# Kernel optimization log

Measured on AMD Instinct MI355X. Metric: run time of the kernel, lower is better.

## Reference

```python
import jax, jax.numpy as jnp
import numpy as np

IMG = 224
WS = 8      # windows_size
STRIDE = 2
M = 1

def _dct_mat(size):
    i = np.arange(size)[:, None]
    j = np.arange(size)[None, :]
    scale = np.where(i == 0, np.sqrt(1.0 / size), np.sqrt(2.0 / size))
    return (scale * np.cos((j + 0.5) * np.pi * i / size)).astype(np.float32)

def _gen_filter(start, end, size):
    i = np.arange(size)[:, None]
    j = np.arange(size)[None, :]
    s = i + j
    return np.where((s > end) | (s < start), 0.0, 1.0).astype(np.float32)

def setup_inputs() -> dict:
    key = jax.random.key(0)
    x = jax.random.normal(key, (16, 3, IMG, IMG), dtype=jnp.float32)
    D = jnp.asarray(_dct_mat(WS))                       # [ws, ws] DCT matrix
    filt = jnp.asarray(_gen_filter(WS // 3, WS * 2, WS))  # high-pass base filter
    return {"x": x, "D": D, "filt": filt}

def reference(x, D, filt):
    b, c, H, W = x.shape
    n = (H - WS) // STRIDE + 1                 # patches per side (109)
    rows = jnp.arange(n)[:, None] * STRIDE + jnp.arange(WS)[None, :]  # [n, ws]
    # unfold: overlapping stride-2 patches -> [b, n, n, c, ws, ws]
    p = x[:, :, rows, :]                       # [b, c, n, ws, W]
    p = p[..., rows]                           # [b, c, n, ws, n, ws]
    p = p.transpose(0, 2, 4, 1, 3, 5)          # [b, n, n, c, ws, ws]
    # block DCT: D @ p @ D^T
    xd = jnp.einsum('pi,bmncij,qj->bmncpq', D, p, D)
    # filter (use_learnable=False, norm=False -> plain elementwise mask)
    y = xd * filt
    # block IDCT: D^T @ y @ D
    y = jnp.einsum('pi,bmncpq,qj->bmncij', D, y, D)
    # fold: overlap-add scatter back to [b, c, H, W]
    hh = rows[:, None, :, None]                # [n,1,ws,1]
    ww = rows[None, :, None, :]                # [1,n,1,ws]
    flat = hh * W + ww                         # [n,n,ws,ws] flat spatial index
    y_t = y.transpose(0, 3, 1, 2, 4, 5)        # [b, c, n, n, ws, ws]
    out = jnp.zeros((b, c, H * W), x.dtype).at[:, :, flat].add(y_t)
    return out.reshape(b, c, H, W)             # m=1 -> cat is identity
```

## Files before the change

kernel.cpp:

```cpp
#include <hip/hip_runtime.h>

#define IMG 224
#define NP 109
#define BC 48
#define NPIX (IMG * IMG)
#define TILE 56
#define QT 28
#define PT 31
#define XR 68
#define XC2 34
#define NTHR 512


#define LOAD_D_SCALARS(D)                                                  \
    const float d0_0 = (D)[0], d0_1 = (D)[1], d0_2 = (D)[2], d0_3 = (D)[3],\
                d0_4 = (D)[4], d0_5 = (D)[5], d0_6 = (D)[6], d0_7 = (D)[7];\
    const float d1_0 = (D)[8],  d1_1 = (D)[9],  d1_2 = (D)[10],            \
                d1_3 = (D)[11], d1_4 = (D)[12], d1_5 = (D)[13],            \
                d1_6 = (D)[14], d1_7 = (D)[15];

#define O_XE   0
#define O_XO   (O_XE + XR * XC2)
#define O_RS   (O_XO + XR * XC2)
#define O_RT   (O_RS + XR * PT)
#define O_RSE  O_RS
#define O_RSO  (O_RSE + PT * QT)
#define O_RTE  (O_RSO + PT * QT)
#define O_RTO  (O_RTE + PT * QT)
#define O_CA   (O_RT + XR * PT)
#define O_CB   (O_CA + PT * PT)
#define O_CC   (O_CB + PT * PT)
#define LDS_FLOATS (O_CC + PT * PT)

__global__ __launch_bounds__(NTHR) void fused_dct_kernel(
    const float* __restrict__ x, const float* __restrict__ D,
    const float* __restrict__ filt, float* __restrict__ out)
{
    __shared__ float lds[LDS_FLOATS];
    float* const xe_s = lds + O_XE;
    float* const xo_s = lds + O_XO;
    float* const rs_s = lds + O_RS;
    float* const rt_s = lds + O_RT;
    float* const ca_s = lds + O_CA;
    float* const cb_s = lds + O_CB;
    float* const cc_s = lds + O_CC;
    float* const RSe  = lds + O_RSE;
    float* const RSo  = lds + O_RSO;
    float* const RTe  = lds + O_RTE;
    float* const RTo  = lds + O_RTO;

    const int tid = threadIdx.x;
    const int h0 = blockIdx.y * TILE;
    const int w0 = blockIdx.x * TILE;
    const int bc = blockIdx.z;

    LOAD_D_SCALARS(D)
    const float w00 = 1.0f - filt[0];
    const float w01 = 1.0f - filt[1];
    const float w10 = 1.0f - filt[8];

    const float* xb = x + (size_t)bc * NPIX;

    for (int i = tid; i < XR * XC2; i += NTHR) {
        int r  = i / XC2;
        int c2 = i - r * XC2;
        int gr = h0 - 6 + r;
        int gc = w0 - 6 + 2 * c2;
        float2 v = make_float2(0.f, 0.f);
        if ((unsigned)gr < (unsigned)IMG && (unsigned)gc < (unsigned)IMG)
            v = *(const float2*)(xb + (size_t)gr * IMG + gc);
        xe_s[r * XC2 + c2] = v.x;
        xo_s[r * XC2 + c2] = v.y;
    }
    __syncthreads();

    for (int i = tid; i < XR * PT; i += NTHR) {
        int r  = i / PT;
        int pc = i - r * PT;
        int b  = r * XC2 + pc;
        float e0 = xe_s[b],     o0 = xo_s[b];
        float e1 = xe_s[b + 1], o1 = xo_s[b + 1];
        float e2 = xe_s[b + 2], o2 = xo_s[b + 2];
        float e3 = xe_s[b + 3], o3 = xo_s[b + 3];
        float s = fmaf(e0, d0_0, fmaf(o0, d0_1,
                  fmaf(e1, d0_2, fmaf(o1, d0_3,
                  fmaf(e2, d0_4, fmaf(o2, d0_5,
                  fmaf(e3, d0_6, o3 * d0_7)))))));
        float t = fmaf(e0, d1_0, fmaf(o0, d1_1,
                  fmaf(e1, d1_2, fmaf(o1, d1_3,
                  fmaf(e2, d1_4, fmaf(o2, d1_5,
                  fmaf(e3, d1_6, o3 * d1_7)))))));
        rs_s[i] = s;
        rt_s[i] = t;
    }
    __syncthreads();

    const int pr0 = (h0 >> 1) - 3;
    const int pc0 = (w0 >> 1) - 3;
    for (int p = tid; p < PT * PT; p += NTHR) {
        int prl = p / PT;
        int pcl = p - prl * PT;
        int b   = (2 * prl) * PT + pcl;
        float c00 = 0.f, c01 = 0.f, c10 = 0.f;
#define P3_ROW(i)                                                              \
        {                                                                      \
            float s = rs_s[b + (i) * PT];                                      \
            float t = rt_s[b + (i) * PT];                                      \
            c00 = fmaf(d0_##i, s, c00);                                        \
            c01 = fmaf(d0_##i, t, c01);                                        \
            c10 = fmaf(d1_##i, s, c10);                                        \
        }
        P3_ROW(0) P3_ROW(1) P3_ROW(2) P3_ROW(3)
        P3_ROW(4) P3_ROW(5) P3_ROW(6) P3_ROW(7)
#undef P3_ROW
        bool valid = ((unsigned)(pr0 + prl) < (unsigned)NP) &&
                     ((unsigned)(pc0 + pcl) < (unsigned)NP);
        float m = valid ? 1.0f : 0.0f;
        ca_s[p] = c00 * w00 * m;
        cb_s[p] = c01 * w01 * m;
        cc_s[p] = c10 * w10 * m;
    }
    __syncthreads();

    for (int i = tid; i < PT * QT; i += NTHR) {
        int pr = i / QT;
        int qw = i - pr * QT;
        int b  = pr * PT + qw;
        float se = 0.f, so = 0.f, te = 0.f, to = 0.f;
#define P4_COL(kc, je, jo)                                                     \
        {                                                                      \
            float a = ca_s[b + (kc)];                                          \
            float bb = cb_s[b + (kc)];                                         \
            float c = cc_s[b + (kc)];                                          \
            se = fmaf(a, d0_##je, fmaf(bb, d1_##je, se));                      \
            so = fmaf(a, d0_##jo, fmaf(bb, d1_##jo, so));                      \
            te = fmaf(c, d0_##je, te);                                         \
            to = fmaf(c, d0_##jo, to);                                         \
        }
        P4_COL(0, 6, 7) P4_COL(1, 4, 5) P4_COL(2, 2, 3) P4_COL(3, 0, 1)
#undef P4_COL
        RSe[i] = se; RSo[i] = so; RTe[i] = te; RTo[i] = to;
    }
    __syncthreads();

    const int qh0 = h0 >> 1, qw0 = w0 >> 1;
    float* ob = out + (size_t)bc * NPIX;
    for (int q = tid; q < QT * QT; q += NTHR) {
        int qhl = q / QT;
        int qwl = q - qhl * QT;
        int b   = qhl * QT + qwl;
        float aee = 0.f, aeo = 0.f, aoe = 0.f, aoo = 0.f;
#define P5_ROW(kr, ie, io)                                                     \
        {                                                                      \
            int o = b + (kr) * QT;                                             \
            float se = RSe[o], so = RSo[o], te = RTe[o], to = RTo[o];          \
            aee = fmaf(d0_##ie, se, fmaf(d1_##ie, te, aee));                   \
            aeo = fmaf(d0_##ie, so, fmaf(d1_##ie, to, aeo));                   \
            aoe = fmaf(d0_##io, se, fmaf(d1_##io, te, aoe));                   \
            aoo = fmaf(d0_##io, so, fmaf(d1_##io, to, aoo));                   \
        }
        P5_ROW(0, 6, 7) P5_ROW(1, 4, 5) P5_ROW(2, 2, 3) P5_ROW(3, 0, 1)
#undef P5_ROW

        int qh = qh0 + qhl, qw = qw0 + qwl;
        int nvr = min(qh, NP - 1) - max(qh - 3, 0) + 1;
        int nvc = min(qw, NP - 1) - max(qw - 3, 0) + 1;
        float cnt = (float)(nvr * nvc);

        int xr = (2 * qhl + 6) * XC2 + (qwl + 3);
        float x00 = xe_s[xr],       x01 = xo_s[xr];
        float x10 = xe_s[xr + XC2], x11 = xo_s[xr + XC2];

        float2 o0, o1;
        o0.x = fmaf(cnt, x00, -aee);
        o0.y = fmaf(cnt, x01, -aeo);
        o1.x = fmaf(cnt, x10, -aoe);
        o1.y = fmaf(cnt, x11, -aoo);

        float* orp = ob + (size_t)(h0 + 2 * qhl) * IMG + (w0 + 2 * qwl);
        *(float2*)orp         = o0;
        *(float2*)(orp + IMG) = o1;
    }
}

extern "C" void kernel_launch(void* const* d_in, const int* in_sizes, int n_in,
                              void* d_out, int out_size, void* d_ws, size_t ws_size,
                              hipStream_t stream)
{
    const float* x    = (const float*)d_in[0];
    const float* D    = (const float*)d_in[1];
    const float* filt = (const float*)d_in[2];
    float* out        = (float*)d_out;

    dim3 grid(IMG / TILE, IMG / TILE, BC);
    fused_dct_kernel<<<grid, NTHR, 0, stream>>>(x, D, filt, out);
    (void)d_ws; (void)ws_size;
}
```

Before: 72.60 us.

## Register-block each stage over four outputs with padded LDS and float4 accesses

Each thread of every separable DCT stage now computes four adjacent outputs instead of one. This reuses the overlapping sliding-window inputs held in registers and lets LDS reads and writes and the global stores use float4. LDS rows are padded to multiples of four floats so those vector accesses stay aligned. It cuts LDS instruction count and address arithmetic, at the cost of more registers per thread and fewer threads active in each stage, which may leave much of the 512-thread block idle.

```diff
diff --git a/kernel.cpp b/kernel.cpp
--- a/kernel.cpp
+++ b/kernel.cpp
@@ -9,6 +9,9 @@
 #define PT 31
 #define XR 68
 #define XC2 34
+#define XCP 36
+#define RSP 32
+#define CAP 32
 #define NTHR 512
 
 
@@ -19,24 +22,28 @@
                 d1_3 = (D)[11], d1_4 = (D)[12], d1_5 = (D)[13],            \
                 d1_6 = (D)[14], d1_7 = (D)[15];
 
+#define DOT8(x0,y0,x1,y1,x2,y2,x3,y3, q0,q1,q2,q3,q4,q5,q6,q7)             \
+    fmaf(x0,q0, fmaf(y0,q1, fmaf(x1,q2, fmaf(y1,q3,                        \
+    fmaf(x2,q4, fmaf(y2,q5, fmaf(x3,q6, (y3)*(q7))))))))
+
 #define O_XE   0
-#define O_XO   (O_XE + XR * XC2)
-#define O_RS   (O_XO + XR * XC2)
-#define O_RT   (O_RS + XR * PT)
+#define O_XO   (O_XE + XR * XCP)
+#define O_RS   (O_XO + XR * XCP)
+#define O_RT   (O_RS + XR * RSP)
 #define O_RSE  O_RS
 #define O_RSO  (O_RSE + PT * QT)
 #define O_RTE  (O_RSO + PT * QT)
 #define O_RTO  (O_RTE + PT * QT)
-#define O_CA   (O_RT + XR * PT)
-#define O_CB   (O_CA + PT * PT)
-#define O_CC   (O_CB + PT * PT)
-#define LDS_FLOATS (O_CC + PT * PT)
+#define O_CA   (O_RT + XR * RSP)
+#define O_CB   (O_CA + PT * CAP)
+#define O_CC   (O_CB + PT * CAP)
+#define LDS_FLOATS (O_CC + PT * CAP)
 
 __global__ __launch_bounds__(NTHR) void fused_dct_kernel(
     const float* __restrict__ x, const float* __restrict__ D,
     const float* __restrict__ filt, float* __restrict__ out)
 {
-    __shared__ float lds[LDS_FLOATS];
+    __shared__ __attribute__((aligned(16))) float lds[LDS_FLOATS];
     float* const xe_s = lds + O_XE;
     float* const xo_s = lds + O_XO;
     float* const rs_s = lds + O_RS;
@@ -69,117 +76,172 @@
         float2 v = make_float2(0.f, 0.f);
         if ((unsigned)gr < (unsigned)IMG && (unsigned)gc < (unsigned)IMG)
             v = *(const float2*)(xb + (size_t)gr * IMG + gc);
-        xe_s[r * XC2 + c2] = v.x;
-        xo_s[r * XC2 + c2] = v.y;
-    }
-    __syncthreads();
-
-    for (int i = tid; i < XR * PT; i += NTHR) {
-        int r  = i / PT;
-        int pc = i - r * PT;
-        int b  = r * XC2 + pc;
-        float e0 = xe_s[b],     o0 = xo_s[b];
-        float e1 = xe_s[b + 1], o1 = xo_s[b + 1];
-        float e2 = xe_s[b + 2], o2 = xo_s[b + 2];
-        float e3 = xe_s[b + 3], o3 = xo_s[b + 3];
-        float s = fmaf(e0, d0_0, fmaf(o0, d0_1,
-                  fmaf(e1, d0_2, fmaf(o1, d0_3,
-                  fmaf(e2, d0_4, fmaf(o2, d0_5,
-                  fmaf(e3, d0_6, o3 * d0_7)))))));
-        float t = fmaf(e0, d1_0, fmaf(o0, d1_1,
-                  fmaf(e1, d1_2, fmaf(o1, d1_3,
-                  fmaf(e2, d1_4, fmaf(o2, d1_5,
-                  fmaf(e3, d1_6, o3 * d1_7)))))));
-        rs_s[i] = s;
-        rt_s[i] = t;
+        xe_s[r * XCP + c2] = v.x;
+        xo_s[r * XCP + c2] = v.y;
+    }
+    __syncthreads();
+
+    for (int i = tid; i < XR * 8; i += NTHR) {
+        int r = i >> 3, g = i & 7;
+        int base = r * XCP + 4 * g;
+        float4 E0 = *(const float4*)(xe_s + base);
+        float4 E1 = *(const float4*)(xe_s + base + 4);
+        float4 O0 = *(const float4*)(xo_s + base);
+        float4 O1 = *(const float4*)(xo_s + base + 4);
+        float e0=E0.x, e1=E0.y, e2=E0.z, e3=E0.w, e4=E1.x, e5=E1.y, e6=E1.z;
+        float o0=O0.x, o1=O0.y, o2=O0.z, o3=O0.w, o4=O1.x, o5=O1.y, o6=O1.z;
+        float s0 = DOT8(e0,o0,e1,o1,e2,o2,e3,o3, d0_0,d0_1,d0_2,d0_3,d0_4,d0_5,d0_6,d0_7);
+        float s1 = DOT8(e1,o1,e2,o2,e3,o3,e4,o4, d0_0,d0_1,d0_2,d0_3,d0_4,d0_5,d0_6,d0_7);
+        float s2 = DOT8(e2,o2,e3,o3,e4,o4,e5,o5, d0_0,d0_1,d0_2,d0_3,d0_4,d0_5,d0_6,d0_7);
+        float s3 = DOT8(e3,o3,e4,o4,e5,o5,e6,o6, d0_0,d0_1,d0_2,d0_3,d0_4,d0_5,d0_6,d0_7);
+        float t0 = DOT8(e0,o0,e1,o1,e2,o2,e3,o3, d1_0,d1_1,d1_2,d1_3,d1_4,d1_5,d1_6,d1_7);
+        float t1 = DOT8(e1,o1,e2,o2,e3,o3,e4,o4, d1_0,d1_1,d1_2,d1_3,d1_4,d1_5,d1_6,d1_7);
+        float t2 = DOT8(e2,o2,e3,o3,e4,o4,e5,o5, d1_0,d1_1,d1_2,d1_3,d1_4,d1_5,d1_6,d1_7);
+        float t3 = DOT8(e3,o3,e4,o4,e5,o5,e6,o6, d1_0,d1_1,d1_2,d1_3,d1_4,d1_5,d1_6,d1_7);
+        *(float4*)(rs_s + r * RSP + 4 * g) = make_float4(s0, s1, s2, s3);
+        *(float4*)(rt_s + r * RSP + 4 * g) = make_float4(t0, t1, t2, t3);
     }
     __syncthreads();
 
     const int pr0 = (h0 >> 1) - 3;
     const int pc0 = (w0 >> 1) - 3;
-    for (int p = tid; p < PT * PT; p += NTHR) {
-        int prl = p / PT;
-        int pcl = p - prl * PT;
-        int b   = (2 * prl) * PT + pcl;
-        float c00 = 0.f, c01 = 0.f, c10 = 0.f;
-#define P3_ROW(i)                                                              \
+    for (int i = tid; i < PT * 8; i += NTHR) {
+        int prl = i >> 3, g = i & 7;
+        int pcb = 4 * g;
+        float c00x=0.f,c00y=0.f,c00z=0.f,c00w=0.f;
+        float c01x=0.f,c01y=0.f,c01z=0.f,c01w=0.f;
+        float c10x=0.f,c10y=0.f,c10z=0.f,c10w=0.f;
+#define P3R(i8)                                                                \
         {                                                                      \
-            float s = rs_s[b + (i) * PT];                                      \
-            float t = rt_s[b + (i) * PT];                                      \
-            c00 = fmaf(d0_##i, s, c00);                                        \
-            c01 = fmaf(d0_##i, t, c01);                                        \
-            c10 = fmaf(d1_##i, s, c10);                                        \
+            const float4 S = *(const float4*)(rs_s + (2*prl+(i8))*RSP + pcb);  \
+            const float4 T = *(const float4*)(rt_s + (2*prl+(i8))*RSP + pcb);  \
+            c00x = fmaf(d0_##i8, S.x, c00x); c00y = fmaf(d0_##i8, S.y, c00y);  \
+            c00z = fmaf(d0_##i8, S.z, c00z); c00w = fmaf(d0_##i8, S.w, c00w);  \
+            c01x = fmaf(d0_##i8, T.x, c01x); c01y = fmaf(d0_##i8, T.y, c01y);  \
+            c01z = fmaf(d0_##i8, T.z, c01z); c01w = fmaf(d0_##i8, T.w, c01w);  \
+            c10x = fmaf(d1_##i8, S.x, c10x); c10y = fmaf(d1_##i8, S.y, c10y);  \
+            c10z = fmaf(d1_##i8, S.z, c10z); c10w = fmaf(d1_##i8, S.w, c10w);  \
         }
-        P3_ROW(0) P3_ROW(1) P3_ROW(2) P3_ROW(3)
-        P3_ROW(4) P3_ROW(5) P3_ROW(6) P3_ROW(7)
-#undef P3_ROW
-        bool valid = ((unsigned)(pr0 + prl) < (unsigned)NP) &&
-                     ((unsigned)(pc0 + pcl) < (unsigned)NP);
-        float m = valid ? 1.0f : 0.0f;
-        ca_s[p] = c00 * w00 * m;
-        cb_s[p] = c01 * w01 * m;
-        cc_s[p] = c10 * w10 * m;
-    }
-    __syncthreads();
-
-    for (int i = tid; i < PT * QT; i += NTHR) {
-        int pr = i / QT;
-        int qw = i - pr * QT;
-        int b  = pr * PT + qw;
-        float se = 0.f, so = 0.f, te = 0.f, to = 0.f;
-#define P4_COL(kc, je, jo)                                                     \
+        P3R(0) P3R(1) P3R(2) P3R(3) P3R(4) P3R(5) P3R(6) P3R(7)
+#undef P3R
+        bool pr_ok = (unsigned)(pr0 + prl) < (unsigned)NP;
+        bool v0 = pr_ok && (pcb+0 < PT) && ((unsigned)(pc0+pcb+0) < (unsigned)NP);
+        bool v1 = pr_ok && (pcb+1 < PT) && ((unsigned)(pc0+pcb+1) < (unsigned)NP);
+        bool v2 = pr_ok && (pcb+2 < PT) && ((unsigned)(pc0+pcb+2) < (unsigned)NP);
+        bool v3 = pr_ok && (pcb+3 < PT) && ((unsigned)(pc0+pcb+3) < (unsigned)NP);
+        *(float4*)(ca_s + prl*CAP + pcb) = make_float4(
+            v0 ? c00x*w00 : 0.f, v1 ? c00y*w00 : 0.f,
+            v2 ? c00z*w00 : 0.f, v3 ? c00w*w00 : 0.f);
+        *(float4*)(cb_s + prl*CAP + pcb) = make_float4(
+            v0 ? c01x*w01 : 0.f, v1 ? c01y*w01 : 0.f,
+            v2 ? c01z*w01 : 0.f, v3 ? c01w*w01 : 0.f);
+        *(float4*)(cc_s + prl*CAP + pcb) = make_float4(
+            v0 ? c10x*w10 : 0.f, v1 ? c10y*w10 : 0.f,
+            v2 ? c10z*w10 : 0.f, v3 ? c10w*w10 : 0.f);
+    }
+    __syncthreads();
+
+#define P4J(A0_,A1_,A2_,A3_, B0_,B1_,B2_,B3_, C0_,C1_,C2_,C3_, SE,SO,TE,TO)   \
+    SE = fmaf(A0_,d0_6, fmaf(B0_,d1_6, fmaf(A1_,d0_4, fmaf(B1_,d1_4,          \
+         fmaf(A2_,d0_2, fmaf(B2_,d1_2, fmaf(A3_,d0_0, (B3_)*d1_0)))))));      \
+    SO = fmaf(A0_,d0_7, fmaf(B0_,d1_7, fmaf(A1_,d0_5, fmaf(B1_,d1_5,          \
+         fmaf(A2_,d0_3, fmaf(B2_,d1_3, fmaf(A3_,d0_1, (B3_)*d1_1)))))));      \
+    TE = fmaf(C0_,d0_6, fmaf(C1_,d0_4, fmaf(C2_,d0_2, (C3_)*d0_0)));          \
+    TO = fmaf(C0_,d0_7, fmaf(C1_,d0_5, fmaf(C2_,d0_3, (C3_)*d0_1)));
+    for (int i = tid; i < PT * 7; i += NTHR) {
+        int pr = i / 7;
+        int qg = i - pr * 7;
+        int qw0 = 4 * qg;
+        int base = pr * CAP + qw0;
+        float4 A0 = *(const float4*)(ca_s + base);
+        float4 A1 = *(const float4*)(ca_s + base + 4);
+        float4 B0 = *(const float4*)(cb_s + base);
+        float4 B1 = *(const float4*)(cb_s + base + 4);
+        float4 C0 = *(const float4*)(cc_s + base);
+        float4 C1 = *(const float4*)(cc_s + base + 4);
+        float a0=A0.x,a1=A0.y,a2=A0.z,a3=A0.w,a4=A1.x,a5=A1.y,a6=A1.z;
+        float b0=B0.x,b1=B0.y,b2=B0.z,b3=B0.w,b4=B1.x,b5=B1.y,b6=B1.z;
+        float c0=C0.x,c1=C0.y,c2=C0.z,c3=C0.w,c4=C1.x,c5=C1.y,c6=C1.z;
+        float se0,so0,te0,to0, se1,so1,te1,to1;
+        float se2,so2,te2,to2, se3,so3,te3,to3;
+        P4J(a0,a1,a2,a3, b0,b1,b2,b3, c0,c1,c2,c3, se0,so0,te0,to0)
+        P4J(a1,a2,a3,a4, b1,b2,b3,b4, c1,c2,c3,c4, se1,so1,te1,to1)
+        P4J(a2,a3,a4,a5, b2,b3,b4,b5, c2,c3,c4,c5, se2,so2,te2,to2)
+        P4J(a3,a4,a5,a6, b3,b4,b5,b6, c3,c4,c5,c6, se3,so3,te3,to3)
+        int o = pr * QT + qw0;
+        *(float4*)(RSe + o) = make_float4(se0, se1, se2, se3);
+        *(float4*)(RSo + o) = make_float4(so0, so1, so2, so3);
+        *(float4*)(RTe + o) = make_float4(te0, te1, te2, te3);
+        *(float4*)(RTo + o) = make_float4(to0, to1, to2, to3);
+    }
+#undef P4J
+    __syncthreads();
+
+    const int qh0 = h0 >> 1, qw0g = w0 >> 1;
+    float* ob = out + (size_t)bc * NPIX;
+    for (int i = tid; i < QT * 7; i += NTHR) {
+        int qhl = i / 7;
+        int qg  = i - qhl * 7;
+        int qwl0 = 4 * qg;
+        float aee0=0.f,aee1=0.f,aee2=0.f,aee3=0.f;
+        float aeo0=0.f,aeo1=0.f,aeo2=0.f,aeo3=0.f;
+        float aoe0=0.f,aoe1=0.f,aoe2=0.f,aoe3=0.f;
+        float aoo0=0.f,aoo1=0.f,aoo2=0.f,aoo3=0.f;
+#define P5R(kr, ie, io)                                                        \
         {                                                                      \
-            float a = ca_s[b + (kc)];                                          \
-            float bb = cb_s[b + (kc)];                                         \
-            float c = cc_s[b + (kc)];                                          \
-            se = fmaf(a, d0_##je, fmaf(bb, d1_##je, se));                      \
-            so = fmaf(a, d0_##jo, fmaf(bb, d1_##jo, so));                      \
-            te = fmaf(c, d0_##je, te);                                         \
-            to = fmaf(c, d0_##jo, to);                                         \
+            const int o = (qhl + (kr)) * QT + qwl0;                            \
+            const float4 SE = *(const float4*)(RSe + o);                       \
+            const float4 SO = *(const float4*)(RSo + o);                       \
+            const float4 TE = *(const float4*)(RTe + o);                       \
+            const float4 TO = *(const float4*)(RTo + o);                       \
+            aee0 = fmaf(d0_##ie, SE.x, fmaf(d1_##ie, TE.x, aee0));             \
+            aee1 = fmaf(d0_##ie, SE.y, fmaf(d1_##ie, TE.y, aee1));             \
+            aee2 = fmaf(d0_##ie, SE.z, fmaf(d1_##ie, TE.z, aee2));             \
+            aee3 = fmaf(d0_##ie, SE.w, fmaf(d1_##ie, TE.w, aee3));             \
+            aeo0 = fmaf(d0_##ie, SO.x, fmaf(d1_##ie, TO.x, aeo0));             \
+            aeo1 = fmaf(d0_##ie, SO.y, fmaf(d1_##ie, TO.y, aeo1));             \
+            aeo2 = fmaf(d0_##ie, SO.z, fmaf(d1_##ie, TO.z, aeo2));             \
+            aeo3 = fmaf(d0_##ie, SO.w, fmaf(d1_##ie, TO.w, aeo3));             \
+            aoe0 = fmaf(d0_##io, SE.x, fmaf(d1_##io, TE.x, aoe0));             \
+            aoe1 = fmaf(d0_##io, SE.y, fmaf(d1_##io, TE.y, aoe1));             \
+            aoe2 = fmaf(d0_##io, SE.z, fmaf(d1_##io, TE.z, aoe2));             \
+            aoe3 = fmaf(d0_##io, SE.w, fmaf(d1_##io, TE.w, aoe3));             \
+            aoo0 = fmaf(d0_##io, SO.x, fmaf(d1_##io, TO.x, aoo0));             \
+            aoo1 = fmaf(d0_##io, SO.y, fmaf(d1_##io, TO.y, aoo1));             \
+            aoo2 = fmaf(d0_##io, SO.z, fmaf(d1_##io, TO.z, aoo2));             \
+            aoo3 = fmaf(d0_##io, SO.w, fmaf(d1_##io, TO.w, aoo3));             \
         }
-        P4_COL(0, 6, 7) P4_COL(1, 4, 5) P4_COL(2, 2, 3) P4_COL(3, 0, 1)
-#undef P4_COL
-        RSe[i] = se; RSo[i] = so; RTe[i] = te; RTo[i] = to;
-    }
-    __syncthreads();
-
-    const int qh0 = h0 >> 1, qw0 = w0 >> 1;
-    float* ob = out + (size_t)bc * NPIX;
-    for (int q = tid; q < QT * QT; q += NTHR) {
-        int qhl = q / QT;
-        int qwl = q - qhl * QT;
-        int b   = qhl * QT + qwl;
-        float aee = 0.f, aeo = 0.f, aoe = 0.f, aoo = 0.f;
-#define P5_ROW(kr, ie, io)                                                     \
-        {                                                                      \
-            int o = b + (kr) * QT;                                             \
-            float se = RSe[o], so = RSo[o], te = RTe[o], to = RTo[o];          \
-            aee = fmaf(d0_##ie, se, fmaf(d1_##ie, te, aee));                   \
-            aeo = fmaf(d0_##ie, so, fmaf(d1_##ie, to, aeo));                   \
-            aoe = fmaf(d0_##io, se, fmaf(d1_##io, te, aoe));                   \
-            aoo = fmaf(d0_##io, so, fmaf(d1_##io, to, aoo));                   \
-        }
-        P5_ROW(0, 6, 7) P5_ROW(1, 4, 5) P5_ROW(2, 2, 3) P5_ROW(3, 0, 1)
-#undef P5_ROW
-
-        int qh = qh0 + qhl, qw = qw0 + qwl;
+        P5R(0, 6, 7) P5R(1, 4, 5) P5R(2, 2, 3) P5R(3, 0, 1)
+#undef P5R
+
+        int qh  = qh0 + qhl;
         int nvr = min(qh, NP - 1) - max(qh - 3, 0) + 1;
-        int nvc = min(qw, NP - 1) - max(qw - 3, 0) + 1;
-        float cnt = (float)(nvr * nvc);
-
-        int xr = (2 * qhl + 6) * XC2 + (qwl + 3);
-        float x00 = xe_s[xr],       x01 = xo_s[xr];
-        float x10 = xe_s[xr + XC2], x11 = xo_s[xr + XC2];
-
-        float2 o0, o1;
-        o0.x = fmaf(cnt, x00, -aee);
-        o0.y = fmaf(cnt, x01, -aeo);
-        o1.x = fmaf(cnt, x10, -aoe);
-        o1.y = fmaf(cnt, x11, -aoo);
-
-        float* orp = ob + (size_t)(h0 + 2 * qhl) * IMG + (w0 + 2 * qwl);
-        *(float2*)orp         = o0;
-        *(float2*)(orp + IMG) = o1;
+        int qwg = qw0g + qwl0;
+        float cn0 = (float)(nvr * (min(qwg+0, NP-1) - max(qwg+0-3, 0) + 1));
+        float cn1 = (float)(nvr * (min(qwg+1, NP-1) - max(qwg+1-3, 0) + 1));
+        float cn2 = (float)(nvr * (min(qwg+2, NP-1) - max(qwg+2-3, 0) + 1));
+        float cn3 = (float)(nvr * (min(qwg+3, NP-1) - max(qwg+3-3, 0) + 1));
+
+        const int xi = (2*qhl + 6) * XCP + (qwl0 + 3);
+        float x00_0 = xe_s[xi+0], x00_1 = xe_s[xi+1], x00_2 = xe_s[xi+2], x00_3 = xe_s[xi+3];
+        float x01_0 = xo_s[xi+0], x01_1 = xo_s[xi+1], x01_2 = xo_s[xi+2], x01_3 = xo_s[xi+3];
+        float x10_0 = xe_s[xi+XCP+0], x10_1 = xe_s[xi+XCP+1], x10_2 = xe_s[xi+XCP+2], x10_3 = xe_s[xi+XCP+3];
+        float x11_0 = xo_s[xi+XCP+0], x11_1 = xo_s[xi+XCP+1], x11_2 = xo_s[xi+XCP+2], x11_3 = xo_s[xi+XCP+3];
+
+        float4 r0a = make_float4(fmaf(cn0, x00_0, -aee0), fmaf(cn0, x01_0, -aeo0),
+                                 fmaf(cn1, x00_1, -aee1), fmaf(cn1, x01_1, -aeo1));
+        float4 r0b = make_float4(fmaf(cn2, x00_2, -aee2), fmaf(cn2, x01_2, -aeo2),
+                                 fmaf(cn3, x00_3, -aee3), fmaf(cn3, x01_3, -aeo3));
+        float4 r1a = make_float4(fmaf(cn0, x10_0, -aoe0), fmaf(cn0, x11_0, -aoo0),
+                                 fmaf(cn1, x10_1, -aoe1), fmaf(cn1, x11_1, -aoo1));
+        float4 r1b = make_float4(fmaf(cn2, x10_2, -aoe2), fmaf(cn2, x11_2, -aoo2),
+                                 fmaf(cn3, x10_3, -aoe3), fmaf(cn3, x11_3, -aoo3));
+
+        float* orp = ob + (size_t)(h0 + 2*qhl) * IMG + (w0 + 2*qwl0);
+        *(float4*)(orp)           = r0a;
+        *(float4*)(orp + 4)       = r0b;
+        *(float4*)(orp + IMG)     = r1a;
+        *(float4*)(orp + IMG + 4) = r1b;
     }
 }
 
```

After: 74.88 us. +3.1%, slower.
